# Optimization experiments

Measured on AMD Instinct MI355X. Metric: run time of the kernel, lower is better.

The kernel has to match this reference:

```python
import jax, jax.numpy as jnp
import numpy as np
import math

B, S, H = 4, 2048, 1024
M = 512          # memory_size
NH = 16          # num_heads
HD = H // NH     # head_dim
HQ = H // 4      # memory buffer feature dim
EPS = 1e-5


def setup_inputs() -> dict:
    key = jax.random.key(0)
    ks = jax.random.split(key, 16)
    s = 0.02
    inp = {
        "hidden_states": jax.random.normal(ks[0], (B, S, H), jnp.float32),
        "memory_buffer": jax.random.normal(ks[1], (B, M, HQ), jnp.float32),
        "memory_mask": jax.random.randint(ks[2], (B, M), 0, 2, jnp.int32),
        "surprise_score": jnp.asarray(0.7, jnp.float32),
        # projections
        "Wq": s * jax.random.normal(ks[3], (H, H), jnp.float32),
        "bq": jnp.zeros((H,), jnp.float32),
        "Wk": s * jax.random.normal(ks[4], (HQ, H), jnp.float32),
        "bk": jnp.zeros((H,), jnp.float32),
        "Wv": s * jax.random.normal(ks[5], (HQ, H), jnp.float32),
        "bv": jnp.zeros((H,), jnp.float32),
        # memory_fusion: Linear(2H,H) -> GELU -> Linear(H,H) -> LayerNorm(H)
        "W1": s * jax.random.normal(ks[6], (2 * H, H), jnp.float32),
        "b1": jnp.zeros((H,), jnp.float32),
        "W2": s * jax.random.normal(ks[7], (H, H), jnp.float32),
        "b2": jnp.zeros((H,), jnp.float32),
        "ln_g": jnp.ones((H,), jnp.float32),
        "ln_b": jnp.zeros((H,), jnp.float32),
        # gate_network: Linear(2H,H) -> GELU -> Linear(H,1) -> Sigmoid
        "Wg1": s * jax.random.normal(ks[8], (2 * H, H), jnp.float32),
        "bg1": jnp.zeros((H,), jnp.float32),
        "Wg2": s * jax.random.normal(ks[9], (H, 1), jnp.float32),
        "bg2": jnp.zeros((1,), jnp.float32),
    }
    return inp


def _layer_norm(x, g, b):
    mu = jnp.mean(x, axis=-1, keepdims=True)
    var = jnp.mean(jnp.square(x - mu), axis=-1, keepdims=True)
    return (x - mu) * jax.lax.rsqrt(var + EPS) * g + b


def reference(hidden_states, memory_buffer, memory_mask, surprise_score,
              Wq, bq, Wk, bk, Wv, bv,
              W1, b1, W2, b2, ln_g, ln_b,
              Wg1, bg1, Wg2, bg2):
    # projections
    q = (hidden_states @ Wq + bq).reshape(B, S, NH, HD)          # [B,S,nh,hd]
    k = (memory_buffer @ Wk + bk).reshape(B, M, NH, HD)          # [B,M,nh,hd]
    v = (memory_buffer @ Wv + bv).reshape(B, M, NH, HD)          # [B,M,nh,hd]

    # masked cross-attention over memory
    logits = jnp.einsum("bsnd,bmnd->bsnm", q, k) / math.sqrt(HD)  # [B,S,nh,M]
    mask = memory_mask[:, None, None, :]                          # [B,1,1,M]
    logits = jnp.where(mask == 0, -jnp.inf, logits)
    weights = jax.nn.softmax(logits, axis=-1)                     # [B,S,nh,M]

    # surprise-based reweight (applied only if surprise_score > 0.6)
    w2 = weights * (1.0 + surprise_score)
    w2 = w2 / jnp.sum(w2, axis=-1, keepdims=True)
    weights = jnp.where(surprise_score > 0.6, w2, weights)

    attended = jnp.einsum("bsnm,bmnd->bsnd", weights, v).reshape(B, S, H)

    combined = jnp.concatenate([hidden_states, attended], axis=-1)  # [B,S,2H]
    fused = _layer_norm(
        jax.nn.gelu(combined @ W1 + b1, approximate=False) @ W2 + b2,
        ln_g, ln_b)                                                 # [B,S,H]
    gate = jax.nn.sigmoid(
        jax.nn.gelu(combined @ Wg1 + bg1, approximate=False) @ Wg2 + bg2)  # [B,S,1]

    out = gate * fused + (1.0 - gate) * hidden_states
    mem_attn = jnp.mean(weights, axis=2)                            # [B,S,M]
    return out, mem_attn
```

## Files before the change

kernel.cpp:

```cpp
#include <hip/hip_runtime.h>
#include <cstdint>
#include <cstdio>

#define B_ 4
#define S_ 2048
#define H_ 1024
#define M_ 512
#define NH_ 16
#define HD_ 64

typedef short bf16x8 __attribute__((ext_vector_type(8)));
typedef float f32x4 __attribute__((ext_vector_type(4)));

__device__ __forceinline__ ushort f2bf(float x) {
  union { float f; uint32_t u; } c; c.f = x;
  uint32_t r = (c.u + 0x7fffu + ((c.u >> 16) & 1u)) >> 16;
  return (ushort)r;
}
__device__ __forceinline__ float bf2f(ushort h) {
  union { uint32_t u; float f; } c; c.u = ((uint32_t)h) << 16;
  return c.f;
}

__global__ __launch_bounds__(256) void cvt_k(
    const float* __restrict__ in, ushort* __restrict__ hi, int n4)
{
  const int i = blockIdx.x * 256 + threadIdx.x;
  if (i >= n4) return;
  const float4 v = ((const float4*)in)[i];
  ushort4 h;
  h.x = f2bf(v.x); h.y = f2bf(v.y); h.z = f2bf(v.z); h.w = f2bf(v.w);
  ((ushort4*)hi)[i] = h;
}

__global__ __launch_bounds__(256) void splitT_k(
    const float* __restrict__ W, ushort* __restrict__ Th, int K, int N)
{
  __shared__ float tile[32][33];
  const int k0 = blockIdx.x * 32, n0 = blockIdx.y * 32;
  const int t = threadIdx.x;
  {
    const int r = t >> 3, c = (t & 7) * 4;
    const float4 v = *(const float4*)&W[(size_t)(k0 + r) * N + n0 + c];
    tile[r][c] = v.x; tile[r][c + 1] = v.y; tile[r][c + 2] = v.z; tile[r][c + 3] = v.w;
  }
  __syncthreads();
  {
    const int n = t >> 3, k = (t & 7) * 4;
    ushort4 h;
    h.x = f2bf(tile[k][n]);
    h.y = f2bf(tile[k + 1][n]);
    h.z = f2bf(tile[k + 2][n]);
    h.w = f2bf(tile[k + 3][n]);
    *(ushort4*)&Th[(size_t)(n0 + n) * K + k0 + k] = h;
  }
}

#define GBM 128
#define GBN 128
#define GBK 64

__global__ __launch_bounds__(256) void gemm_bf16s(
    const ushort* __restrict__ A1h, const ushort* __restrict__ A2h,
    const ushort* __restrict__ A1l, const ushort* __restrict__ A2l,
    int asplit, int lda1, int lda2,
    const ushort* __restrict__ Bth, int ldb,
    const float* __restrict__ bias, const float* __restrict__ bias2,
    const int* __restrict__ maskp,
    float* __restrict__ Cf, ushort* __restrict__ Ch, ushort* __restrict__ Cl,
    int ldc,
    long sAb, long sAn, long sBb, long sBn, long sCb, long sCn,
    int K, int nreg, int mode)
{
  __shared__ ushort Ast[GBM * GBK];
  __shared__ ushort Bst[GBN * GBK];

  const int bz = (int)blockIdx.z;
  const int zb = bz >> 4, zn = bz & 15;
  {
    const size_t oA = (size_t)zb * sAb + (size_t)zn * sAn;
    A1h += oA; A1l += oA; A2h += oA; A2l += oA;
    const size_t oB = (size_t)zb * sBb + (size_t)zn * sBn;
    Bth += oB;
    const size_t oC = (size_t)zb * sCb + (size_t)zn * sCn;
    if (Cf) Cf += oC;
    if (Ch) Ch += oC;
    if (Cl) Cl += oC;
  }
  const int* maskb = maskp ? (maskp + zb * M_) : maskp;

  const int t = threadIdx.x;
  const int w = t >> 6, lane = t & 63;
  const int wr = w >> 1, wc = w & 1;

  const int gx = gridDim.x, gy = gridDim.y;
  const int nwg = gx * gy;
  const int bid = (int)(blockIdx.y * gx + blockIdx.x);
  const int swz = (bid & 7) * (nwg >> 3) + (bid >> 3);
  const int bm = (swz / gy) * GBM;
  const int bn = (swz % gy) * GBN;

  f32x4 acc[4][4];
  const f32x4 zero = {0.f, 0.f, 0.f, 0.f};
  #pragma unroll
  for (int i = 0; i < 4; i++)
    #pragma unroll
    for (int j = 0; j < 4; j++) acc[i][j] = zero;

  const int srow = lane >> 3;
  const int sp = lane & 7;
  const int ss = sp ^ srow;
  const int nsteps = (nreg * K) / GBK;

  int reg = 0, kr0 = 0;
  for (int step = 0; step < nsteps; ++step) {
    const ushort* As1 = reg ? A1l : A1h;
    const ushort* As2 = reg ? A2l : A2h;
    const int ke = kr0 + ss * 8;

    #pragma unroll
    for (int i = 0; i < 4; i++) {
      const int rl = w * 32 + i * 8 + srow;
      const ushort* ap = (ke < asplit)
          ? As1 + (size_t)(bm + rl) * lda1 + ke
          : As2 + (size_t)(bm + rl) * lda2 + (ke - asplit);
      __builtin_amdgcn_global_load_lds(
          (const __attribute__((address_space(1))) void*)ap,
          (__attribute__((address_space(3))) void*)&Ast[(w * 32 + i * 8) * GBK],
          16, 0, 0);
      const ushort* bp = Bth + (size_t)(bn + rl) * ldb + ke;
      __builtin_amdgcn_global_load_lds(
          (const __attribute__((address_space(1))) void*)bp,
          (__attribute__((address_space(3))) void*)&Bst[(w * 32 + i * 8) * GBK],
          16, 0, 0);
    }
    __syncthreads();

    #pragma unroll
    for (int ks = 0; ks < 2; ks++) {
      bf16x8 af[4], bfr[4];
      const int kq = ks * 4 + (lane >> 4);
      #pragma unroll
      for (int mi = 0; mi < 4; mi++) {
        const int r = wr * 64 + mi * 16 + (lane & 15);
        af[mi] = *(const bf16x8*)&Ast[r * GBK + ((kq ^ (r & 7)) * 8)];
      }
      #pragma unroll
      for (int ni = 0; ni < 4; ni++) {
        const int r = wc * 64 + ni * 16 + (lane & 15);
        bfr[ni] = *(const bf16x8*)&Bst[r * GBK + ((kq ^ (r & 7)) * 8)];
      }
      #pragma unroll
      for (int mi = 0; mi < 4; mi++)
        #pragma unroll
        for (int ni = 0; ni < 4; ni++)
          acc[mi][ni] = __builtin_amdgcn_mfma_f32_16x16x32_bf16(
              af[mi], bfr[ni], acc[mi][ni], 0, 0, 0);
    }
    __syncthreads();

    kr0 += GBK;
    if (kr0 == K) { kr0 = 0; reg++; }
  }

  #pragma unroll
  for (int ni = 0; ni < 4; ni++) {
    const int col = bn + wc * 64 + ni * 16 + (lane & 15);
    float bv;
    if (mode == 4) bv = 0.f;
    else if ((mode == 5 || mode == 7) && col >= 1024) bv = bias2[col - 1024];
    else bv = bias[col];
    const int mk = (mode == 4) ? maskb[col] : 1;
    #pragma unroll
    for (int mi = 0; mi < 4; mi++) {
      #pragma unroll
      for (int r = 0; r < 4; r++) {
        const int row = bm + wr * 64 + mi * 16 + (lane >> 4) * 4 + r;
        float v = acc[mi][ni][r] + bv;
        const size_t idx = (size_t)row * ldc + col;
        if (mode == 4) {
          const float e = mk ? __expf(v * 0.125f) : 0.f;
          Ch[idx] = f2bf(e);
        } else if (mode == 5) {
          v = 0.5f * v * (1.f + erff(v * 0.70710678f));
          if (col < 1024) {
            Ch[(size_t)row * 1024 + col] = f2bf(v);
          } else {
            Cf[(size_t)row * 1024 + (col - 1024)] = v;
          }
        } else if (mode == 6) {
          Ch[idx] = f2bf(v);
        } else if (mode == 7) {
          if (col < 1024) {
            Ch[(size_t)row * 1024 + col] = f2bf(v);
          } else {
            const int c2 = col - 1024, n = c2 >> 6, d = c2 & 63;
            const int bb = row >> 9, m = row & 511;
            Cl[(((size_t)(bb * 16 + n)) * 64 + d) * 512 + m] = f2bf(v);
          }
        } else {
          Cf[idx] = v;
        }
      }
    }
  }
}

#define PBM 128
#define PBK 64

__global__ __launch_bounds__(256) void gemm_pv(
    const ushort* __restrict__ Eh, const ushort* __restrict__ VTh,
    const float* __restrict__ rsinv, ushort* __restrict__ attH)
{
  __shared__ ushort Ast[PBM * PBK];
  __shared__ ushort Bst[64 * PBK];

  const int bz = (int)blockIdx.z;
  const int b = bz >> 4, n = bz & 15;
  const ushort* E  = Eh  + (size_t)bz * ((size_t)S_ * M_);
  const ushort* Vh = VTh + (size_t)bz * (64 * M_);
  const float*  rs = rsinv + (size_t)bz * S_;
  ushort* CH = attH + (size_t)b * S_ * H_ + n * 64;

  const int t = threadIdx.x;
  const int w = t >> 6, lane = t & 63;

  const int bid = (int)blockIdx.x;
  const int swz = (bid & 7) * 2 + (bid >> 3);
  const int bm = swz * PBM;

  f32x4 acc[2][4];
  const f32x4 zero = {0.f, 0.f, 0.f, 0.f};
  #pragma unroll
  for (int i = 0; i < 2; i++)
    #pragma unroll
    for (int j = 0; j < 4; j++) acc[i][j] = zero;

  const int srow = lane >> 3;
  const int ss = (lane & 7) ^ srow;

  for (int kr0 = 0; kr0 < M_; kr0 += PBK) {
    const int ke = kr0 + ss * 8;

    #pragma unroll
    for (int i = 0; i < 4; i++) {
      const int rl = w * 32 + i * 8 + srow;
      __builtin_amdgcn_global_load_lds(
          (const __attribute__((address_space(1))) void*)(E + (size_t)(bm + rl) * M_ + ke),
          (__attribute__((address_space(3))) void*)&Ast[(w * 32 + i * 8) * PBK],
          16, 0, 0);
    }
    #pragma unroll
    for (int i = 0; i < 2; i++) {
      const int rl = w * 16 + i * 8 + srow;
      __builtin_amdgcn_global_load_lds(
          (const __attribute__((address_space(1))) void*)(Vh + (size_t)rl * M_ + ke),
          (__attribute__((address_space(3))) void*)&Bst[(w * 16 + i * 8) * PBK],
          16, 0, 0);
    }
    __syncthreads();

    #pragma unroll
    for (int ks = 0; ks < 2; ks++) {
      bf16x8 af[2], bfr[4];
      const int kq = ks * 4 + (lane >> 4);
      #pragma unroll
      for (int mi = 0; mi < 2; mi++) {
        const int r = w * 32 + mi * 16 + (lane & 15);
        af[mi] = *(const bf16x8*)&Ast[r * PBK + ((kq ^ (r & 7)) * 8)];
      }
      #pragma unroll
      for (int ni = 0; ni < 4; ni++) {
        const int r = ni * 16 + (lane & 15);
        bfr[ni] = *(const bf16x8*)&Bst[r * PBK + ((kq ^ (r & 7)) * 8)];
      }
      #pragma unroll
      for (int mi = 0; mi < 2; mi++)
        #pragma unroll
        for (int ni = 0; ni < 4; ni++)
          acc[mi][ni] = __builtin_amdgcn_mfma_f32_16x16x32_bf16(
              af[mi], bfr[ni], acc[mi][ni], 0, 0, 0);
    }
    __syncthreads();
  }

  #pragma unroll
  for (int ni = 0; ni < 4; ni++) {
    const int col = ni * 16 + (lane & 15);
    #pragma unroll
    for (int mi = 0; mi < 2; mi++) {
      #pragma unroll
      for (int r = 0; r < 4; r++) {
        const int row = bm + w * 32 + mi * 16 + (lane >> 4) * 4 + r;
        const float v = acc[mi][ni][r] * rs[row];
        CH[(size_t)row * H_ + col] = f2bf(v);
      }
    }
  }
}

__global__ __launch_bounds__(256) void rowmemo_k(
    const ushort* __restrict__ Eh, float* __restrict__ rsinv,
    float* __restrict__ memo)
{
  __shared__ float red[16][17];
  __shared__ float invs[16];
  __shared__ float macc[16][513];
  const int blk = (int)blockIdx.x;
  const int b = blk >> 11, s = blk & 2047;
  const int t = threadIdx.x;
  const int n = t >> 4, seg = (t & 15) * 32;

  float vals[32];
  {
    const ushort* Er = Eh + ((size_t)(b * 16 + n) * S_ + s) * M_ + seg;
    float sum = 0.f;
    #pragma unroll
    for (int j = 0; j < 32; j += 4) {
      const ushort4 u = *(const ushort4*)(Er + j);
      vals[j]     = bf2f(u.x); vals[j + 1] = bf2f(u.y);
      vals[j + 2] = bf2f(u.z); vals[j + 3] = bf2f(u.w);
      sum += vals[j] + vals[j + 1] + vals[j + 2] + vals[j + 3];
    }
    red[n][t & 15] = sum;
  }
  __syncthreads();
  if (t < 16) {
    float sm = 0.f;
    #pragma unroll
    for (int j = 0; j < 16; j++) sm += red[t][j];
    const float inv = 1.f / sm;
    invs[t] = inv;
    rsinv[(size_t)(b * 16 + t) * S_ + s] = inv;
  }
  __syncthreads();
  {
    const float iv = invs[n] * 0.0625f;
    #pragma unroll
    for (int j = 0; j < 32; j++) macc[n][seg + j] = vals[j] * iv;
  }
  __syncthreads();
  {
    const int m0 = 2 * t;
    float a0 = 0.f, a1 = 0.f;
    #pragma unroll
    for (int n2 = 0; n2 < 16; n2++) {
      a0 += macc[n2][m0];
      a1 += macc[n2][m0 + 1];
    }
    float2 o; o.x = a0; o.y = a1;
    *(float2*)&memo[((size_t)(b * S_ + s)) * M_ + m0] = o;
  }
}

__global__ __launch_bounds__(256) void final_k(
    const float* __restrict__ g1, const float* __restrict__ wg2,
    const float* __restrict__ bg2, const float* __restrict__ fp,
    const float* __restrict__ hs, const float* __restrict__ lngm,
    const float* __restrict__ lnbv, float* __restrict__ out)
{
  __shared__ float red[3][256];
  const int r = blockIdx.x, t = threadIdx.x;
  float x[4]; float dotp = 0.f, s1 = 0.f, s2 = 0.f;
  #pragma unroll
  for (int i = 0; i < 4; i++) {
    int c = t + i * 256;
    dotp += g1[(size_t)r * H_ + c] * wg2[c];
    float fv = fp[(size_t)r * H_ + c];
    x[i] = fv; s1 += fv; s2 += fv * fv;
  }
  red[0][t] = dotp; red[1][t] = s1; red[2][t] = s2;
  __syncthreads();
  for (int s = 128; s > 0; s >>= 1) {
    if (t < s) {
      red[0][t] += red[0][t + s];
      red[1][t] += red[1][t + s];
      red[2][t] += red[2][t + s];
    }
    __syncthreads();
  }
  const float gate = 1.f / (1.f + expf(-(red[0][0] + bg2[0])));
  const float mu = red[1][0] * (1.f / 1024.f);
  const float var = red[2][0] * (1.f / 1024.f) - mu * mu;
  const float rs = rsqrtf(var + 1e-5f);
  #pragma unroll
  for (int i = 0; i < 4; i++) {
    int c = t + i * 256;
    float fused = (x[i] - mu) * rs * lngm[c] + lnbv[c];
    float hv = hs[(size_t)r * H_ + c];
    out[(size_t)r * H_ + c] = gate * fused + (1.f - gate) * hv;
  }
}

extern "C" void kernel_launch(void* const* d_in, const int* in_sizes, int n_in,
                              void* d_out, int out_size, void* d_ws, size_t ws_size,
                              hipStream_t stream) {
  const float* hs   = (const float*)d_in[0];
  const float* memb = (const float*)d_in[1];
  const int*   mask = (const int*)d_in[2];
  const float* Wq  = (const float*)d_in[4];  const float* bq  = (const float*)d_in[5];
  const float* Wk  = (const float*)d_in[6];  const float* bk  = (const float*)d_in[7];
  const float* Wv  = (const float*)d_in[8];  const float* bv  = (const float*)d_in[9];
  const float* W1  = (const float*)d_in[10]; const float* b1  = (const float*)d_in[11];
  const float* W2  = (const float*)d_in[12]; const float* b2  = (const float*)d_in[13];
  const float* lng = (const float*)d_in[14]; const float* lnb = (const float*)d_in[15];
  const float* Wg1 = (const float*)d_in[16]; const float* bg1 = (const float*)d_in[17];
  const float* Wg2 = (const float*)d_in[18]; const float* bg2 = (const float*)d_in[19];

  char* ws = (char*)d_ws;
  size_t o = 0;
  auto alloc = [&](size_t bytes) {
    char* p = ws + o; o += (bytes + 255) & ~(size_t)255; return p;
  };
  const size_t NEL   = (size_t)B_ * S_ * H_;
  const size_t EHALF = (size_t)2 * NH_ * S_ * M_;

  ushort* hsH  = (ushort*)alloc(NEL * 2);
  ushort* qH   = (ushort*)alloc(NEL * 2);
  ushort* membH = (ushort*)alloc((size_t)524288 * 2);
  ushort* kH   = (ushort*)alloc((size_t)2097152 * 2);
  ushort* VTh  = (ushort*)alloc((size_t)2097152 * 2);
  ushort* Ebuf = (ushort*)alloc(EHALF * 2);
  float*  rsinv = (float*)alloc((size_t)B_ * NH_ * S_ * 4);
  ushort* WqTh = (ushort*)alloc((size_t)1048576 * 2);
  ushort* WfTh = (ushort*)alloc((size_t)4194304 * 2);
  ushort* W2Th = (ushort*)alloc((size_t)1048576 * 2);
  ushort* WkvT = (ushort*)alloc((size_t)524288 * 2);
  if (o > ws_size) { fprintf(stderr, "ws too small: %zu > %zu\n", o, ws_size); return; }

  ushort* attH = qH;
  ushort* h1H  = Ebuf;
  float*  g1b  = (float*)(Ebuf + NEL);
  float*  fpb  = (float*)hsH;

  float* out  = (float*)d_out;
  float* memo = out + NEL;

  splitT_k<<<dim3(32, 32), 256, 0, stream>>>(Wq, WqTh, 1024, 1024);
  splitT_k<<<dim3(64, 32), 256, 0, stream>>>(W1, WfTh, 2048, 1024);
  splitT_k<<<dim3(64, 32), 256, 0, stream>>>(Wg1, WfTh + (size_t)1024 * 2048, 2048, 1024);
  splitT_k<<<dim3(32, 32), 256, 0, stream>>>(W2, W2Th, 1024, 1024);
  splitT_k<<<dim3(8, 32), 256, 0, stream>>>(Wk, WkvT, 256, 1024);
  splitT_k<<<dim3(8, 32), 256, 0, stream>>>(Wv, WkvT + (size_t)1024 * 256, 256, 1024);
  cvt_k<<<dim3(8192), 256, 0, stream>>>(hs, hsH, 2097152);
  cvt_k<<<dim3(512), 256, 0, stream>>>(memb, membH, 131072);

  gemm_bf16s<<<dim3(16, 16, 1), 256, 0, stream>>>(
      membH, membH, membH, membH, 256, 256, 256, WkvT, 256,
      bk, bv, nullptr, nullptr, kH, VTh, 1024,
      0, 0, 0, 0, 0, 0, 256, 1, 7);

  gemm_bf16s<<<dim3(64, 8, 1), 256, 0, stream>>>(
      hsH, hsH, hsH, hsH, 1024, 1024, 1024, WqTh, 1024,
      bq, nullptr, nullptr, nullptr, qH, nullptr, 1024,
      0, 0, 0, 0, 0, 0, 1024, 1, 6);

  for (int bh = 0; bh < 2; ++bh) {
    const size_t qo = (size_t)bh * 2 * S_ * H_;
    const size_t ko = (size_t)bh * 2 * M_ * H_;
    const size_t vo = (size_t)bh * 2 * NH_ * 64 * M_;
    const size_t ro = (size_t)bh * 2 * NH_ * S_;
    const size_t mo = (size_t)bh * 2 * S_ * M_;

    gemm_bf16s<<<dim3(16, 4, 32), 256, 0, stream>>>(
        qH + qo, qH + qo, qH + qo, qH + qo, 64, 1024, 1024,
        kH + ko, 1024,
        nullptr, nullptr, mask + (size_t)bh * 2 * M_,
        nullptr, Ebuf, nullptr, 512,
        (long)S_ * H_, 64, (long)M_ * H_, 64,
        (long)NH_ * S_ * M_, (long)S_ * M_, 64, 1, 4);

    rowmemo_k<<<dim3(4096), 256, 0, stream>>>(Ebuf, rsinv + ro, memo + mo);

    gemm_pv<<<dim3(16, 1, 32), 256, 0, stream>>>(
        Ebuf, VTh + vo, rsinv + ro, attH + qo);
  }

  gemm_bf16s<<<dim3(64, 16, 1), 256, 0, stream>>>(
      hsH, attH, hsH, attH, 1024, 1024, 1024, WfTh, 2048,
      b1, bg1, nullptr, g1b, h1H, nullptr, 1024,
      0, 0, 0, 0, 0, 0, 2048, 1, 5);

  gemm_bf16s<<<dim3(64, 8, 1), 256, 0, stream>>>(
      h1H, h1H, h1H, h1H, 1024, 1024, 1024, W2Th, 1024,
      b2, nullptr, nullptr, fpb, nullptr, nullptr, 1024,
      0, 0, 0, 0, 0, 0, 1024, 1, 0);

  final_k<<<dim3(8192), 256, 0, stream>>>(g1b, Wg2, bg2, fpb, hs, lng, lnb, out);
}
```

Measured before the change: 556.6 us.

## Double-buffer LDS in bf16 GEMM with 32-wide K steps and new swizzle

The main GEMM kernel now stages K tiles of 32 into two LDS buffers and prefetches the next tile through global_load_lds before computing on the current one. This removes one barrier per step and overlaps global loads with MFMA work. The unused lo-precision operand pointers and the nreg loop are dropped, and the LDS layout uses a new 4-way rotate swizzle. K steps halve in size, so there are twice as many barriers per unit of K, and the loads stay in flight with no explicit vmcnt wait before the barrier.

```diff
diff --git a/kernel.cpp b/kernel.cpp
--- a/kernel.cpp
+++ b/kernel.cpp
@@ -11,6 +11,9 @@
 
 typedef short bf16x8 __attribute__((ext_vector_type(8)));
 typedef float f32x4 __attribute__((ext_vector_type(4)));
+
+#define AS1 __attribute__((address_space(1)))
+#define AS3 __attribute__((address_space(3)))
 
 __device__ __forceinline__ ushort f2bf(float x) {
   union { float f; uint32_t u; } c; c.f = x;
@@ -58,11 +61,9 @@
 
 #define GBM 128
 #define GBN 128
-#define GBK 64
 
 __global__ __launch_bounds__(256) void gemm_bf16s(
     const ushort* __restrict__ A1h, const ushort* __restrict__ A2h,
-    const ushort* __restrict__ A1l, const ushort* __restrict__ A2l,
     int asplit, int lda1, int lda2,
     const ushort* __restrict__ Bth, int ldb,
     const float* __restrict__ bias, const float* __restrict__ bias2,
@@ -70,16 +71,16 @@
     float* __restrict__ Cf, ushort* __restrict__ Ch, ushort* __restrict__ Cl,
     int ldc,
     long sAb, long sAn, long sBb, long sBn, long sCb, long sCn,
-    int K, int nreg, int mode)
-{
-  __shared__ ushort Ast[GBM * GBK];
-  __shared__ ushort Bst[GBN * GBK];
+    int K, int mode)
+{
+  __shared__ ushort Ast[2][4096];
+  __shared__ ushort Bst[2][4096];
 
   const int bz = (int)blockIdx.z;
   const int zb = bz >> 4, zn = bz & 15;
   {
     const size_t oA = (size_t)zb * sAb + (size_t)zn * sAn;
-    A1h += oA; A1l += oA; A2h += oA; A2l += oA;
+    A1h += oA; A2h += oA;
     const size_t oB = (size_t)zb * sBb + (size_t)zn * sBn;
     Bth += oB;
     const size_t oC = (size_t)zb * sCb + (size_t)zn * sCn;
@@ -90,8 +91,8 @@
   const int* maskb = maskp ? (maskp + zb * M_) : maskp;
 
   const int t = threadIdx.x;
-  const int w = t >> 6, lane = t & 63;
-  const int wr = w >> 1, wc = w & 1;
+  const int wv = t >> 6, lane = t & 63;
+  const int wr = wv >> 1, wc = wv & 1;
 
   const int gx = gridDim.x, gy = gridDim.y;
   const int nwg = gx * gy;
@@ -107,61 +108,66 @@
     #pragma unroll
     for (int j = 0; j < 4; j++) acc[i][j] = zero;
 
-  const int srow = lane >> 3;
-  const int sp = lane & 7;
-  const int ss = sp ^ srow;
-  const int nsteps = (nreg * K) / GBK;
-
-  int reg = 0, kr0 = 0;
+  const int swl = lane >> 2;
+  const int sko = ((((lane & 3) - swl) & 3)) * 8;
+  const int ar0 = wv * 16 + swl;
+  const int ar1 = ar0 + 64;
+  const size_t a0r1 = (size_t)(bm + ar0) * lda1;
+  const size_t a0r2 = (size_t)(bm + ar0) * lda2;
+  const size_t a1r1 = (size_t)(bm + ar1) * lda1;
+  const size_t a1r2 = (size_t)(bm + ar1) * lda2;
+  const size_t b0r  = (size_t)(bn + ar0) * ldb;
+  const size_t b1r  = (size_t)(bn + ar1) * ldb;
+
+  const int l15 = lane & 15, kq = lane >> 4;
+  const int rbase = l15 * 32 + ((kq + l15) & 3) * 8;
+
+  const int nsteps = K / 32;
+
+#define STAGE_STEP(bsel, kr0_) do {                                           \
+    const int kr0s = (kr0_);                                                  \
+    const ushort *ab0, *ab1;                                                  \
+    if (kr0s < asplit) {                                                      \
+      ab0 = A1h + a0r1 + kr0s + sko;                                          \
+      ab1 = A1h + a1r1 + kr0s + sko;                                          \
+    } else {                                                                  \
+      ab0 = A2h + a0r2 + (kr0s - asplit) + sko;                               \
+      ab1 = A2h + a1r2 + (kr0s - asplit) + sko;                               \
+    }                                                                         \
+    __builtin_amdgcn_global_load_lds((const AS1 void*)ab0,                    \
+        (AS3 void*)&Ast[bsel][wv * 512], 16, 0, 0);                           \
+    __builtin_amdgcn_global_load_lds((const AS1 void*)ab1,                    \
+        (AS3 void*)&Ast[bsel][(wv + 4) * 512], 16, 0, 0);                     \
+    __builtin_amdgcn_global_load_lds((const AS1 void*)(Bth + b0r + kr0s + sko), \
+        (AS3 void*)&Bst[bsel][wv * 512], 16, 0, 0);                           \
+    __builtin_amdgcn_global_load_lds((const AS1 void*)(Bth + b1r + kr0s + sko), \
+        (AS3 void*)&Bst[bsel][(wv + 4) * 512], 16, 0, 0);                     \
+  } while (0)
+
+  STAGE_STEP(0, 0);
+  __syncthreads();
+
   for (int step = 0; step < nsteps; ++step) {
-    const ushort* As1 = reg ? A1l : A1h;
-    const ushort* As2 = reg ? A2l : A2h;
-    const int ke = kr0 + ss * 8;
-
-    #pragma unroll
-    for (int i = 0; i < 4; i++) {
-      const int rl = w * 32 + i * 8 + srow;
-      const ushort* ap = (ke < asplit)
-          ? As1 + (size_t)(bm + rl) * lda1 + ke
-          : As2 + (size_t)(bm + rl) * lda2 + (ke - asplit);
-      __builtin_amdgcn_global_load_lds(
-          (const __attribute__((address_space(1))) void*)ap,
-          (__attribute__((address_space(3))) void*)&Ast[(w * 32 + i * 8) * GBK],
-          16, 0, 0);
-      const ushort* bp = Bth + (size_t)(bn + rl) * ldb + ke;
-      __builtin_amdgcn_global_load_lds(
-          (const __attribute__((address_space(1))) void*)bp,
-          (__attribute__((address_space(3))) void*)&Bst[(w * 32 + i * 8) * GBK],
-          16, 0, 0);
-    }
+    const int cur = step & 1;
+    if (step + 1 < nsteps) STAGE_STEP(cur ^ 1, (step + 1) * 32);
+
+    bf16x8 af[4], bfr[4];
+    #pragma unroll
+    for (int mi = 0; mi < 4; mi++)
+      af[mi] = *(const bf16x8*)&Ast[cur][(wr * 4 + mi) * 512 + rbase];
+    #pragma unroll
+    for (int ni = 0; ni < 4; ni++)
+      bfr[ni] = *(const bf16x8*)&Bst[cur][(wc * 4 + ni) * 512 + rbase];
+    #pragma unroll
+    for (int mi = 0; mi < 4; mi++)
+      #pragma unroll
+      for (int ni = 0; ni < 4; ni++)
+        acc[mi][ni] = __builtin_amdgcn_mfma_f32_16x16x32_bf16(
+            af[mi], bfr[ni], acc[mi][ni], 0, 0, 0);
+
     __syncthreads();
-
-    #pragma unroll
-    for (int ks = 0; ks < 2; ks++) {
-      bf16x8 af[4], bfr[4];
-      const int kq = ks * 4 + (lane >> 4);
-      #pragma unroll
-      for (int mi = 0; mi < 4; mi++) {
-        const int r = wr * 64 + mi * 16 + (lane & 15);
-        af[mi] = *(const bf16x8*)&Ast[r * GBK + ((kq ^ (r & 7)) * 8)];
-      }
-      #pragma unroll
-      for (int ni = 0; ni < 4; ni++) {
-        const int r = wc * 64 + ni * 16 + (lane & 15);
-        bfr[ni] = *(const bf16x8*)&Bst[r * GBK + ((kq ^ (r & 7)) * 8)];
-      }
-      #pragma unroll
-      for (int mi = 0; mi < 4; mi++)
-        #pragma unroll
-        for (int ni = 0; ni < 4; ni++)
-          acc[mi][ni] = __builtin_amdgcn_mfma_f32_16x16x32_bf16(
-              af[mi], bfr[ni], acc[mi][ni], 0, 0, 0);
-    }
-    __syncthreads();
-
-    kr0 += GBK;
-    if (kr0 == K) { kr0 = 0; reg++; }
-  }
+  }
+#undef STAGE_STEP
 
   #pragma unroll
   for (int ni = 0; ni < 4; ni++) {
@@ -247,17 +253,15 @@
     for (int i = 0; i < 4; i++) {
       const int rl = w * 32 + i * 8 + srow;
       __builtin_amdgcn_global_load_lds(
-          (const __attribute__((address_space(1))) void*)(E + (size_t)(bm + rl) * M_ + ke),
-          (__attribute__((address_space(3))) void*)&Ast[(w * 32 + i * 8) * PBK],
-          16, 0, 0);
+          (const AS1 void*)(E + (size_t)(bm + rl) * M_ + ke),
+          (AS3 void*)&Ast[(w * 32 + i * 8) * PBK], 16, 0, 0);
     }
     #pragma unroll
     for (int i = 0; i < 2; i++) {
       const int rl = w * 16 + i * 8 + srow;
       __builtin_amdgcn_global_load_lds(
-          (const __attribute__((address_space(1))) void*)(Vh + (size_t)rl * M_ + ke),
-          (__attribute__((address_space(3))) void*)&Bst[(w * 16 + i * 8) * PBK],
-          16, 0, 0);
+          (const AS1 void*)(Vh + (size_t)rl * M_ + ke),
+          (AS3 void*)&Bst[(w * 16 + i * 8) * PBK], 16, 0, 0);
     }
     __syncthreads();
 
@@ -447,14 +451,14 @@
   cvt_k<<<dim3(512), 256, 0, stream>>>(memb, membH, 131072);
 
   gemm_bf16s<<<dim3(16, 16, 1), 256, 0, stream>>>(
-      membH, membH, membH, membH, 256, 256, 256, WkvT, 256,
+      membH, membH, 256, 256, 256, WkvT, 256,
       bk, bv, nullptr, nullptr, kH, VTh, 1024,
-      0, 0, 0, 0, 0, 0, 256, 1, 7);
+      0, 0, 0, 0, 0, 0, 256, 7);
 
   gemm_bf16s<<<dim3(64, 8, 1), 256, 0, stream>>>(
-      hsH, hsH, hsH, hsH, 1024, 1024, 1024, WqTh, 1024,
+      hsH, hsH, 1024, 1024, 1024, WqTh, 1024,
       bq, nullptr, nullptr, nullptr, qH, nullptr, 1024,
-      0, 0, 0, 0, 0, 0, 1024, 1, 6);
+      0, 0, 0, 0, 0, 0, 1024, 6);
 
   for (int bh = 0; bh < 2; ++bh) {
     const size_t qo = (size_t)bh * 2 * S_ * H_;
@@ -464,12 +468,12 @@
     const size_t mo = (size_t)bh * 2 * S_ * M_;
 
     gemm_bf16s<<<dim3(16, 4, 32), 256, 0, stream>>>(
-        qH + qo, qH + qo, qH + qo, qH + qo, 64, 1024, 1024,
+        qH + qo, qH + qo, 64, 1024, 1024,
         kH + ko, 1024,
         nullptr, nullptr, mask + (size_t)bh * 2 * M_,
         nullptr, Ebuf, nullptr, 512,
         (long)S_ * H_, 64, (long)M_ * H_, 64,
-        (long)NH_ * S_ * M_, (long)S_ * M_, 64, 1, 4);
+        (long)NH_ * S_ * M_, (long)S_ * M_, 64, 4);
 
     rowmemo_k<<<dim3(4096), 256, 0, stream>>>(Ebuf, rsinv + ro, memo + mo);
 
@@ -478,14 +482,14 @@
   }
 
   gemm_bf16s<<<dim3(64, 16, 1), 256, 0, stream>>>(
-      hsH, attH, hsH, attH, 1024, 1024, 1024, WfTh, 2048,
+      hsH, attH, 1024, 1024, 1024, WfTh, 2048,
       b1, bg1, nullptr, g1b, h1H, nullptr, 1024,
-      0, 0, 0, 0, 0, 0, 2048, 1, 5);
+      0, 0, 0, 0, 0, 0, 2048, 5);
 
   gemm_bf16s<<<dim3(64, 8, 1), 256, 0, stream>>>(
-      h1H, h1H, h1H, h1H, 1024, 1024, 1024, W2Th, 1024,
+      h1H, h1H, 1024, 1024, 1024, W2Th, 1024,
       b2, nullptr, nullptr, fpb, nullptr, nullptr, 1024,
-      0, 0, 0, 0, 0, 0, 1024, 1, 0);
+      0, 0, 0, 0, 0, 0, 1024, 0);
 
   final_k<<<dim3(8192), 256, 0, stream>>>(g1b, Wg2, bg2, fpb, hs, lng, lnb, out);
 }
```

After: 552.3 us. No clear change (-0.8%).
